# Optimization experiments

Hardware: AMD Instinct MI355X
Metric: run time of the kernel (lower is better)

## Reference

```python
import jax, jax.numpy as jnp
import numpy as np
from jax import lax

T, B = 32, 32
GRID = (16, 16)
N_ACT = 5
CNN_DIM = 512
MAP_DIM = CNN_DIM + N_ACT  # 517
FLAT = MAP_DIM * GRID[0] * GRID[1]  # 132352


def _conv(x, w, b, stride):
    y = lax.conv_general_dilated(x, w, (stride, stride), 'VALID',
                                 dimension_numbers=('NCHW', 'OIHW', 'NCHW'))
    return jax.nn.relu(y + b[None, :, None, None])


def setup_inputs() -> dict:
    key = jax.random.key(0)
    ks = jax.random.split(key, 16)
    inp = {
        'image': jax.random.uniform(ks[0], (T * B, 3, 64, 64), jnp.float32),
        'last_action': jax.random.randint(ks[1], (T * B,), 0, N_ACT),
        'position': jax.random.randint(ks[2], (T * B, 2), 0, GRID[0]),
        'done': jnp.zeros((T, B), jnp.float32),
        'state0': jnp.zeros((B, MAP_DIM, GRID[0], GRID[1]), jnp.float32),
        'c1_w': jax.random.normal(ks[3], (32, 3, 8, 8), jnp.float32) * 0.05,
        'c1_b': jnp.zeros((32,), jnp.float32),
        'c2_w': jax.random.normal(ks[4], (64, 32, 4, 4), jnp.float32) * 0.05,
        'c2_b': jnp.zeros((64,), jnp.float32),
        'c3_w': jax.random.normal(ks[5], (64, 64, 3, 3), jnp.float32) * 0.05,
        'c3_b': jnp.zeros((64,), jnp.float32),
        'fc_w': jax.random.normal(ks[6], (CNN_DIM, 1024), jnp.float32) * 0.03,
        'fc_b': jnp.zeros((CNN_DIM,), jnp.float32),
        'pol_w1': jax.random.normal(ks[7], (64, FLAT), jnp.float32) * 0.005,
        'pol_b1': jnp.zeros((64,), jnp.float32),
        'pol_w2': jax.random.normal(ks[8], (N_ACT, 64), jnp.float32) * 0.01,
        'pol_b2': jnp.zeros((N_ACT,), jnp.float32),
        'val_w1': jax.random.normal(ks[9], (64, FLAT), jnp.float32) * 0.005,
        'val_b1': jnp.zeros((64,), jnp.float32),
        'val_w2': jax.random.normal(ks[10], (1, 64), jnp.float32) * 0.01,
        'val_b2': jnp.zeros((1,), jnp.float32),
    }
    return inp


def reference(image, last_action, position, done, state0,
              c1_w, c1_b, c2_w, c2_b, c3_w, c3_b, fc_w, fc_b,
              pol_w1, pol_b1, pol_w2, pol_b2, val_w1, val_b1, val_w2, val_b2):
    # NatureCNN feature extractor (image already normalized to [0,1])
    x = _conv(image, c1_w, c1_b, 4)   # (TB,32,15,15)
    x = _conv(x, c2_w, c2_b, 2)       # (TB,64,6,6)
    x = _conv(x, c3_w, c3_b, 1)       # (TB,64,4,4)
    feat = jax.nn.relu(x.reshape(x.shape[0], -1) @ fc_w.T + fc_b)  # (TB,512)
    onehot = jax.nn.one_hot(last_action, N_ACT, dtype=feat.dtype)
    h = jnp.concatenate([feat, onehot], axis=1)       # (TB,517)

    h_seq = h.reshape(T, B, MAP_DIM)
    idx_seq = position.reshape(T, B, 2)
    benv = jnp.arange(B)

    def step(state, inp):
        ht, dt, it = inp
        masked = (1.0 - dt)[:, None, None, None] * state      # reset done envs
        new_state = masked.at[benv, :, it[:, 0], it[:, 1]].set(ht)  # scatter write
        return new_state, new_state.reshape(B, -1)

    final_state, outs = lax.scan(step, state0, (h_seq, done, idx_seq))
    hidden = outs.reshape(T * B, FLAT)

    logits = jnp.tanh(hidden @ pol_w1.T + pol_b1) @ pol_w2.T + pol_b2  # (TB,5)
    v = jnp.tanh(hidden @ val_w1.T + val_b1) @ val_w2.T + val_b2       # (TB,1)
    return logits, v, final_state
```

## Files before the change

kernel.cpp:

```cpp
#include <hip/hip_runtime.h>

#define T_ 32
#define B_ 32
#define MAPD 517
#define P_ 256
#define FLATD (MAPD*P_)
#define TBN (T_*B_)

typedef unsigned short u16;
typedef unsigned int u32;
typedef __attribute__((ext_vector_type(4))) short short4v;
typedef __attribute__((ext_vector_type(8))) short short8v;
typedef __attribute__((ext_vector_type(4))) float f32x4;
typedef __attribute__((ext_vector_type(2))) float f32x2;
typedef __attribute__((ext_vector_type(4))) u32 u32x4;

__device__ __forceinline__ float bfv(u16 u){ u32 x = ((u32)u)<<16; return __uint_as_float(x); }
__device__ __forceinline__ u16 fbf(float f){
  u32 x = __float_as_uint(f);
  return (u16)((x + 0x7fffu + ((x>>16)&1u))>>16);
}
template<bool F32> __device__ __forceinline__ float ld(const void* p, size_t i){
  if constexpr (F32) return ((const float*)p)[i];
  else               return bfv(((const u16*)p)[i]);
}
__device__ __forceinline__ float ldf(bool f32, const void* p, size_t i){
  return f32 ? ((const float*)p)[i] : bfv(((const u16*)p)[i]);
}

__device__ __forceinline__ bool probe_f32(const void* img){
  int lane = threadIdx.x & 63;
  ushort4 v = ((const ushort4*)img)[lane];
  int c = (v.x <= 0x4380u) + (v.y <= 0x4380u) + (v.z <= 0x4380u) + (v.w <= 0x4380u);
  #pragma unroll
  for (int off = 32; off > 0; off >>= 1) c += __shfl_xor(c, off, 64);
  return c < 240;
}

template<bool F32> __device__ void wt_body(int lbid, const void* pw1, const void* vw1,
                                           u16* wt, u32* tile){
  int c  = lbid >> 1;
  int ph = lbid & 1;
  for (int half = 0; half < 2; ++half){
    for (int it = 0; it < 2; ++it){
      int idx = it*256 + threadIdx.x;
      int jp = idx >> 3, pgl = idx & 7;
      int j0 = jp*2;
      const void* w = (j0 < 64) ? pw1 : vw1;
      int jj0 = (j0 < 64) ? j0 : j0-64;
      size_t base0 = (size_t)jj0*FLATD + c*P_ + ph*128 + half*64 + pgl*8;
      size_t base1 = base0 + FLATD;
      u16 a[8], b[8];
      if constexpr (F32){
        const float* f = (const float*)w;
        float4 a0 = *(const float4*)(f + base0), a1 = *(const float4*)(f + base0 + 4);
        float4 b0 = *(const float4*)(f + base1), b1 = *(const float4*)(f + base1 + 4);
        a[0]=fbf(a0.x); a[1]=fbf(a0.y); a[2]=fbf(a0.z); a[3]=fbf(a0.w);
        a[4]=fbf(a1.x); a[5]=fbf(a1.y); a[6]=fbf(a1.z); a[7]=fbf(a1.w);
        b[0]=fbf(b0.x); b[1]=fbf(b0.y); b[2]=fbf(b0.z); b[3]=fbf(b0.w);
        b[4]=fbf(b1.x); b[5]=fbf(b1.y); b[6]=fbf(b1.z); b[7]=fbf(b1.w);
      } else {
        short8v va = *(const short8v*)((const u16*)w + base0);
        short8v vb = *(const short8v*)((const u16*)w + base1);
        #pragma unroll
        for (int k = 0; k < 8; ++k){ a[k] = (u16)va[k]; b[k] = (u16)vb[k]; }
      }
      int slot = (jp >> 2) ^ (half*8 + pgl);
      int sub  = jp & 3;
      #pragma unroll
      for (int k = 0; k < 8; ++k){
        int ppl = pgl*8 + k;
        tile[ppl*64 + slot*4 + sub] = (u32)a[k] | ((u32)b[k] << 16);
      }
    }
    __syncthreads();
    for (int it = 0; it < 4; ++it){
      int idx = it*256 + threadIdx.x;
      int ppl = idx >> 4, jb = idx & 15;
      int slot = jb ^ (half*8 + (ppl >> 3));
      u32x4 v = *(const u32x4*)(tile + ppl*64 + slot*4);
      int p = ph*128 + half*64 + ppl;
      *(u32x4*)(wt + ((size_t)p*MAPD + c)*128 + jb*8) = v;
    }
    __syncthreads();
  }
}

__device__ void prep_body(bool f32, int bid, const void* c1w, const void* c2w, const void* c3w,
                          const void* fcw, const void* st0,
                          u16* W1F, u16* W2F, u16* W3F, u16* FWF, u16* ST0T, char* smem_){
  int tid = threadIdx.x;
  if (bid < 24){
    int idx = bid*256 + tid;
    int j = idx & 7, l = (idx>>3) & 63, t = idx>>9;
    int nt = t/6, s = t - nt*6;
    int oc = nt*16 + (l&15);
    int kk = 8*(4*s + (l>>4)) + j;
    float v = ldf(f32, c1w, oc*192+kk);
    W1F[idx] = fbf(v);
  } else if (bid < 152){
    int idx = (bid-24)*256 + tid;
    int j = idx & 7, l = (idx>>3) & 63, s = (idx>>9) & 15, nt = idx>>13;
    int oc = nt*16 + (l&15);
    int cin = (l>>4)*8 + j;
    int src = oc*512 + cin*16 + (s>>2)*4 + (s&3);
    W2F[idx] = fbf(ldf(f32, c2w, src));
  } else if (bid < 296){
    int idx = (bid-152)*256 + tid;
    int j = idx & 7, l = (idx>>3) & 63, t = idx>>9;
    int nt = t/18, s = t - nt*18;
    int oc = nt*16 + (l&15);
    int c = (s&1)*32 + (l>>4)*8 + j;
    int src = oc*576 + c*9 + (s>>1);
    W3F[idx] = fbf(ldf(f32, c3w, src));
  } else if (bid < 328){
    u16* tile = (u16*)smem_;
    int nt = bid - 296;
    int ol = tid >> 4;
    int o  = nt*16 + ol;
    for (int par = 0; par < 2; ++par){
      for (int it = 0; it < 2; ++it){
        int m = par*32 + it*16 + (tid & 15);
        int col = (((m>>3)&3)*16 + ol)*8 + (m&7);
        u16 v[16];
        if (f32){
          const float* f = (const float*)fcw + (size_t)o*1024 + 16*m;
          #pragma unroll
          for (int q = 0; q < 4; ++q){
            float4 x = *(const float4*)(f + q*4);
            v[q*4+0]=fbf(x.x); v[q*4+1]=fbf(x.y); v[q*4+2]=fbf(x.z); v[q*4+3]=fbf(x.w);
          }
        } else {
          const u16* f = (const u16*)fcw + (size_t)o*1024 + 16*m;
          short8v x0 = *(const short8v*)f;
          short8v x1 = *(const short8v*)(f + 8);
          #pragma unroll
          for (int q = 0; q < 8; ++q){ v[q] = (u16)x0[q]; v[8+q] = (u16)x1[q]; }
        }
        #pragma unroll
        for (int r = 0; r < 16; ++r)
          tile[r*512 + col] = v[r];
      }
      __syncthreads();
      for (int it = 0; it < 4; ++it){
        int idx = it*256 + tid;
        int row = idx >> 6, colv = idx & 63;
        u32x4 w = *(const u32x4*)((const u32*)tile + row*256 + colv*4);
        int frag = nt*32 + row*2 + par;
        *(u32x4*)(FWF + (size_t)frag*512 + colv*8) = w;
      }
      __syncthreads();
    }
  } else {
    u16* tile = (u16*)smem_;
    int b0 = bid - 328;
    int c0 = (b0 >> 2)*8, p0 = (b0 & 3)*64;
    for (int half = 0; half < 2; ++half){
      int ch = c0 + half*4;
      for (int it = 0; it < 4; ++it){
        int idx = it*256 + tid;
        int pg = idx & 7, b = (idx>>3) & 31, ci = idx >> 8;
        int c = ch + ci;
        u16 v[8];
        if (c < MAPD){
          size_t src = ((size_t)b*MAPD + c)*256 + p0 + pg*8;
          if (f32){
            const float* f = (const float*)st0;
            float4 x0 = *(const float4*)(f + src), x1 = *(const float4*)(f + src + 4);
            v[0]=fbf(x0.x); v[1]=fbf(x0.y); v[2]=fbf(x0.z); v[3]=fbf(x0.w);
            v[4]=fbf(x1.x); v[5]=fbf(x1.y); v[6]=fbf(x1.z); v[7]=fbf(x1.w);
          } else {
            short8v x = *(const short8v*)((const u16*)st0 + src);
            #pragma unroll
            for (int k = 0; k < 8; ++k) v[k] = (u16)x[k];
          }
        } else {
          #pragma unroll
          for (int k = 0; k < 8; ++k) v[k] = 0;
        }
        #pragma unroll
        for (int kk = 0; kk < 8; ++kk){
          int k2 = (kk + pg) & 7;
          tile[ci*2304 + (pg*8 + k2)*36 + b] = v[k2];
        }
      }
      __syncthreads();
      for (int it = 0; it < 8; ++it){
        int idx = it*256 + tid;
        int bq = idx & 7, pl = (idx>>3) & 63, ci = idx >> 9;
        int c = ch + ci;
        if (c < MAPD){
          ushort4 v = *(const ushort4*)(tile + ci*2304 + pl*36 + bq*4);
          *(ushort4*)(ST0T + ((size_t)(p0+pl)*MAPD + c)*32 + bq*4) = v;
        }
      }
      __syncthreads();
    }
  }
}

__device__ void meta_body(bool f32, int bid, const int* pos, const void* done, const int* lact,
                          int* prev, float* coef, float* H, int* lastw, float* lastc){
  if (bid < 4){
    int i = bid*256 + threadIdx.x;
    int t = i >> 5, b = i & 31;
    int p = pos[i*2]*16 + pos[i*2+1];
    int pv = -1;
    for (int s = t-1; s >= 0; --s){
      int n = s*32 + b;
      if (pos[n*2]*16 + pos[n*2+1] == p){ pv = s; break; }
    }
    float cf = 1.f;
    for (int s = (pv<0?0:pv+1); s <= t-1; ++s)
      cf *= (1.f - ldf(f32, done, s*32+b));
    prev[i] = pv; coef[i] = cf;
    int la = lact[i];
    #pragma unroll
    for (int a = 0; a < 5; ++a) H[(size_t)i*MAPD + 512 + a] = (la == a) ? 1.f : 0.f;
  } else {
    int i = (bid-4)*256 + threadIdx.x;
    int b = i >> 8, p = i & 255;
    int lw = -1;
    for (int s = T_-1; s >= 0; --s){
      int n = s*32 + b;
      if (pos[n*2]*16 + pos[n*2+1] == p){ lw = s; break; }
    }
    float cf = 1.f;
    for (int s = (lw<0?0:lw+1); s < T_; ++s)
      cf *= (1.f - ldf(f32, done, s*32+b));
    lastw[i] = lw; lastc[i] = cf;
  }
}

__global__ __launch_bounds__(256) void k_A(const void* image,
                                           const void* pw1, const void* vw1, u16* wt,
                                           const void* c1w, const void* c2w, const void* c3w,
                                           const void* fcw, const void* st0,
                                           u16* W1F, u16* W2F, u16* W3F, u16* FWF, u16* ST0T,
                                           const int* pos, const void* done, const int* lact,
                                           int* prev, float* coef, float* H, int* lastw, float* lastc){
  __shared__ __align__(16) char smem_[18464];
  bool f32 = probe_f32(image);
  int bid = blockIdx.x;
  if (bid < 1034){
    if (f32) wt_body<true>(bid, pw1, vw1, wt, (u32*)smem_);
    else     wt_body<false>(bid, pw1, vw1, wt, (u32*)smem_);
  } else if (bid < 1622){
    prep_body(f32, bid-1034, c1w, c2w, c3w, fcw, st0, W1F, W2F, W3F, FWF, ST0T, smem_);
  } else {
    meta_body(f32, bid-1622, pos, done, lact, prev, coef, H, lastw, lastc);
  }
}

__global__ __launch_bounds__(256) void k_conv123(const void* img,
                                                 const u16* __restrict__ W1F, const void* b1,
                                                 const u16* __restrict__ W2F, const void* b2,
                                                 const u16* __restrict__ W3F, const void* b3,
                                                 u16* __restrict__ out){
  __shared__ __align__(16) u16 smem[19488];
  u16* sImg = smem;
  u16* sA   = smem + 12288;
  u16* sBv  = smem;
  bool f32 = probe_f32(img);
  int n = blockIdx.x, tid = threadIdx.x;
  if (f32){
    const float4* ip = (const float4*)((const float*)img + (size_t)n*12288);
    for (int i = tid; i < 3072; i += 256){
      float4 v = ip[i];
      ushort4 u; u.x = fbf(v.x); u.y = fbf(v.y); u.z = fbf(v.z); u.w = fbf(v.w);
      int L = i*4;
      int addr = (L & ~63) | (((L & 63) + (((L >> 6) & 3) << 4)) & 63);
      *(ushort4*)(sImg + addr) = u;
    }
  } else {
    const ushort4* ip = (const ushort4*)((const u16*)img + (size_t)n*12288);
    for (int i = tid; i < 3072; i += 256){
      ushort4 u = ip[i];
      int L = i*4;
      int addr = (L & ~63) | (((L & 63) + (((L >> 6) & 3) << 4)) & 63);
      *(ushort4*)(sImg + addr) = u;
    }
  }
  int wv = tid >> 6, lane = tid & 63;
  int mi = lane & 15, q = lane >> 4;

  short8v bfr1[2][6];
  #pragma unroll
  for (int nt = 0; nt < 2; ++nt)
    #pragma unroll
    for (int s = 0; s < 6; ++s)
      bfr1[nt][s] = ((const short8v*)W1F)[(nt*6+s)*64 + lane];
  float b1v[2];
  #pragma unroll
  for (int nt = 0; nt < 2; ++nt)
    b1v[nt] = ldf(f32, b1, nt*16+mi);
  __syncthreads();

  {
    f32x4 acc[4][2];
    #pragma unroll
    for (int mt = 0; mt < 4; ++mt)
      #pragma unroll
      for (int nt = 0; nt < 2; ++nt)
        acc[mt][nt] = (f32x4){0.f,0.f,0.f,0.f};
    int base[4];
    #pragma unroll
    for (int mt = 0; mt < 4; ++mt){
      int m = (wv*4+mt)*16 + mi;
      int mc = m < 225 ? m : 224;
      int oy = mc/15, ox = mc - oy*15;
      base[mt] = oy*256 + ox*4;
    }
    for (int s = 0; s < 6; ++s){
      int cky = 4*s + q;
      int off = (cky >> 3)*4096 + (cky & 7)*64;
      #pragma unroll
      for (int mt = 0; mt < 4; ++mt){
        int Lb = base[mt] + off;
        const u16* rp = sImg + (Lb & ~63);
        int x0 = Lb & 63;
        int rot = ((Lb >> 6) & 3) << 4;
        short4v lo = *(const short4v*)(rp + ((x0 + rot) & 63));
        short4v hi = *(const short4v*)(rp + ((x0 + 4 + rot) & 63));
        short8v a = __builtin_shufflevector(lo, hi, 0,1,2,3,4,5,6,7);
        acc[mt][0] = __builtin_amdgcn_mfma_f32_16x16x32_bf16(a, bfr1[0][s], acc[mt][0], 0,0,0);
        acc[mt][1] = __builtin_amdgcn_mfma_f32_16x16x32_bf16(a, bfr1[1][s], acc[mt][1], 0,0,0);
      }
    }
    __syncthreads();
    #pragma unroll
    for (int mt = 0; mt < 4; ++mt){
      int mrow0 = (wv*4+mt)*16 + q*4;
      #pragma unroll
      for (int nt = 0; nt < 2; ++nt){
        int oc = nt*16 + mi;
        #pragma unroll
        for (int r = 0; r < 4; ++r){
          int m = mrow0 + r;
          if (m < 225){
            int g = ((oc >> 3) ^ ((m >> 1) & 3)) << 3;
            sA[m*32 + g + (oc & 7)] = fbf(fmaxf(acc[mt][nt][r] + b1v[nt], 0.f));
          }
        }
      }
    }
  }
  __syncthreads();

  {
    short8v bfr2[16];
    #pragma unroll
    for (int s = 0; s < 16; ++s)
      bfr2[s] = ((const short8v*)W2F)[(wv*16+s)*64 + lane];
    int oc = wv*16 + mi;
    float bv = ldf(f32, b2, oc);
    f32x4 acc[3];
    #pragma unroll
    for (int mt = 0; mt < 3; ++mt) acc[mt] = (f32x4){0.f,0.f,0.f,0.f};
    int pixb[3];
    #pragma unroll
    for (int mt = 0; mt < 3; ++mt){
      int m = mt*16 + mi; if (m > 35) m = 35;
      int oy = m/6, ox = m - oy*6;
      pixb[mt] = oy*30 + ox*2;
    }
    #pragma unroll
    for (int s = 0; s < 16; ++s){
      int dp = (s>>2)*15 + (s&3);
      #pragma unroll
      for (int mt = 0; mt < 3; ++mt){
        int pix = pixb[mt] + dp;
        int g = (q ^ ((pix >> 1) & 3)) << 3;
        short8v a = *(const short8v*)(sA + pix*32 + g);
        acc[mt] = __builtin_amdgcn_mfma_f32_16x16x32_bf16(a, bfr2[s], acc[mt], 0,0,0);
      }
    }
    __syncthreads();
    #pragma unroll
    for (int mt = 0; mt < 3; ++mt)
      #pragma unroll
      for (int r = 0; r < 4; ++r){
        int m = mt*16 + q*4 + r;
        if (m < 36){
          int g = ((oc >> 3) ^ (m & 7)) << 3;
          sBv[m*64 + g + (oc & 7)] = fbf(fmaxf(acc[mt][r] + bv, 0.f));
        }
      }
  }
  __syncthreads();

  {
    int oy = mi >> 2, ox = mi & 3;
    int oc = wv*16 + mi;
    float bv = ldf(f32, b3, oc);
    short8v bfr3[18];
    #pragma unroll
    for (int s = 0; s < 18; ++s)
      bfr3[s] = ((const short8v*)W3F)[(wv*18+s)*64 + lane];
    f32x4 acc = (f32x4){0.f,0.f,0.f,0.f};
    #pragma unroll
    for (int s = 0; s < 18; ++s){
      int pair = s >> 1, ky = pair/3, kx = pair - ky*3;
      int pix = (oy+ky)*6 + ox+kx;
      int g = ((((s & 1) << 2) | q) ^ (pix & 7)) << 3;
      short8v a = *(const short8v*)(sBv + pix*64 + g);
      acc = __builtin_amdgcn_mfma_f32_16x16x32_bf16(a, bfr3[s], acc, 0,0,0);
    }
    u16* ob = out + (size_t)n*1024;
    #pragma unroll
    for (int r = 0; r < 4; ++r)
      ob[(q*4+r)*64 + oc] = fbf(fmaxf(acc[r] + bv, 0.f));
  }
}

template<int CLEN>
__device__ __forceinline__ void yloop(const u16* __restrict__ wp, const float* __restrict__ sSb,
                                      float (&acc)[8][2]){
  #pragma unroll 10
  for (int c = 0; c < CLEN; ++c){
    u32 w = *(const u32*)(wp + (size_t)c*128);
    float w0 = bfv((u16)(w & 0xffffu)), w1 = bfv((u16)(w >> 16));
    const float4* s4 = (const float4*)(sSb + c*32);
    float4 sa = s4[0], sb = s4[1];
    float sv[8] = {sa.x,sa.y,sa.z,sa.w,sb.x,sb.y,sb.z,sb.w};
    #pragma unroll
    for (int bb = 0; bb < 8; ++bb){
      acc[bb][0] += sv[bb]*w0;
      acc[bb][1] += sv[bb]*w1;
    }
  }
}
__device__ void yinit_body(int lbid, const u16* __restrict__ ST0T, const u16* __restrict__ wt,
                           u16* __restrict__ PARTB, float* sS){
  int p = lbid >> 2, cq = lbid & 3;
  int c0 = cq*130;
  int clen = (cq == 3) ? 127 : 130;
  const ushort4* ssrc = (const ushort4*)(ST0T + ((size_t)p*MAPD + c0)*32);
  int n4 = clen*8;
  for (int i = threadIdx.x; i < n4; i += 256){
    ushort4 u = ssrc[i];
    float4 f; f.x = bfv(u.x); f.y = bfv(u.y); f.z = bfv(u.z); f.w = bfv(u.w);
    *(float4*)(sS + i*4) = f;
  }
  __syncthreads();
  int jg = threadIdx.x & 63, bg = threadIdx.x >> 6;
  int j0 = jg*2, b0 = bg*8;
  const u16* wp = wt + ((size_t)p*MAPD + c0)*128 + j0;
  float acc[8][2] = {};
  if (cq < 3) yloop<130>(wp, sS + b0, acc);
  else        yloop<127>(wp, sS + b0, acc);
  u32* op = (u32*)(PARTB + (size_t)lbid*4096);
  #pragma unroll
  for (int bb = 0; bb < 8; ++bb){
    u32 pk = (u32)fbf(acc[bb][0]) | ((u32)fbf(acc[bb][1]) << 16);
    op[((b0+bb)*128 + j0) >> 1] = pk;
  }
}
__device__ void fc_body(int lbid, bool f32, const u16* __restrict__ C, const u16* __restrict__ FWF,
                        const void* fb, float* __restrict__ H){
  int wv = threadIdx.x >> 6, lane = threadIdx.x & 63;
  int mi = lane & 15, q = lane >> 4;
  int mt = lbid >> 3;
  int nt = (lbid & 7)*4 + wv;
  const u16* ap = C + (size_t)(mt*16 + mi)*1024 + q*8;
  const short8v* bp = (const short8v*)FWF + (size_t)nt*32*64 + lane;
  f32x4 acc0 = (f32x4){0.f,0.f,0.f,0.f};
  f32x4 acc1 = (f32x4){0.f,0.f,0.f,0.f};
  #pragma unroll
  for (int kt = 0; kt < 32; kt += 2){
    short8v a0 = *(const short8v*)(ap + kt*32);
    short8v b0 = bp[kt*64];
    short8v a1 = *(const short8v*)(ap + (kt+1)*32);
    short8v b1 = bp[(kt+1)*64];
    acc0 = __builtin_amdgcn_mfma_f32_16x16x32_bf16(a0, b0, acc0, 0,0,0);
    acc1 = __builtin_amdgcn_mfma_f32_16x16x32_bf16(a1, b1, acc1, 0,0,0);
  }
  int o = nt*16 + mi;
  float bv = ldf(f32, fb, o);
  #pragma unroll
  for (int r = 0; r < 4; ++r){
    int m = mt*16 + q*4 + r;
    H[(size_t)m*MAPD + o] = fmaxf(acc0[r] + acc1[r] + bv, 0.f);
  }
}
__global__ __launch_bounds__(256) void k_C(const void* image,
                                           const u16* __restrict__ ST0T, const u16* __restrict__ wt,
                                           u16* __restrict__ PARTB,
                                           const u16* __restrict__ C, const u16* __restrict__ FWF,
                                           const void* fb, float* __restrict__ H){
  __shared__ float sS[130*32];
  if (blockIdx.x < 1024){
    yinit_body(blockIdx.x, ST0T, wt, PARTB, sS);
  } else {
    bool f32 = probe_f32(image);
    fc_body(blockIdx.x - 1024, f32, C, FWF, fb, H);
  }
}

__device__ void delta_body(int obid, int ltid, float* diff, bool f32,
                           const float* __restrict__ H, const u16* __restrict__ wt,
                           const u16* __restrict__ st0t,
                           const int* __restrict__ pos, const void* done,
                           const int* __restrict__ prev, const float* __restrict__ coef,
                           float* __restrict__ dlt8){
  int n = obid >> 2, cq = obid & 3;
  int c0 = cq*130, clen = (cq == 3) ? 127 : 130;
  int b = n & 31;
  int p = pos[n*2]*16 + pos[n*2+1];
  float dn = ldf(f32, done, n);
  float m = 1.f - dn;
  int pv = prev[n];
  float cf = coef[n]*m;
  const float* hc = H + (size_t)n*MAPD + c0;
  for (int c = ltid; c < clen; c += 128){
    float old;
    if (pv >= 0) old = H[(size_t)(pv*32 + b)*MAPD + c0 + c];
    else         old = bfv(st0t[((size_t)p*MAPD + c0 + c)*32 + b]);
    diff[c] = hc[c] - cf*old;
  }
  __syncthreads();
  int half = ltid >> 6, jp = ltid & 63, j0 = jp*2;
  int hbase, hlen;
  if (cq == 3){ hbase = half*64; hlen = half ? 63 : 64; }
  else        { hbase = half*65; hlen = 65; }
  const u16* wp = wt + ((size_t)p*MAPD + c0 + hbase)*128 + j0;
  const float* dptr = diff + hbase;
  float a0 = 0.f, a1 = 0.f;
  int c = 0;
  for (; c + 4 <= hlen; c += 4){
    u32 w0 = *(const u32*)(wp + (size_t)(c+0)*128);
    u32 w1 = *(const u32*)(wp + (size_t)(c+1)*128);
    u32 w2 = *(const u32*)(wp + (size_t)(c+2)*128);
    u32 w3 = *(const u32*)(wp + (size_t)(c+3)*128);
    float d0 = dptr[c], d1 = dptr[c+1], d2 = dptr[c+2], d3 = dptr[c+3];
    a0 += d0*bfv((u16)(w0 & 0xffffu)) + d1*bfv((u16)(w1 & 0xffffu))
        + d2*bfv((u16)(w2 & 0xffffu)) + d3*bfv((u16)(w3 & 0xffffu));
    a1 += d0*bfv((u16)(w0 >> 16)) + d1*bfv((u16)(w1 >> 16))
        + d2*bfv((u16)(w2 >> 16)) + d3*bfv((u16)(w3 >> 16));
  }
  for (; c < hlen; ++c){
    u32 w = *(const u32*)(wp + (size_t)c*128);
    a0 += dptr[c]*bfv((u16)(w & 0xffffu));
    a1 += dptr[c]*bfv((u16)(w >> 16));
  }
  f32x2 st; st[0] = a0; st[1] = a1;
  *(f32x2*)(dlt8 + ((size_t)obid*2 + half)*128 + j0) = st;
}
__global__ __launch_bounds__(256) void k_D(const void* image,
                                           const float* __restrict__ H, const u16* __restrict__ wt,
                                           const u16* __restrict__ st0t,
                                           const int* __restrict__ pos, const void* done,
                                           const int* __restrict__ prev, const float* __restrict__ coef,
                                           float* __restrict__ dlt8,
                                           const u16* __restrict__ PARTB, float* __restrict__ YI){
  __shared__ float diff2[2][132];
  __shared__ float red[256];
  if (blockIdx.x < 2048){
    bool f32 = probe_f32(image);
    int sub = threadIdx.x >> 7;
    int obid = blockIdx.x*2 + sub;
    delta_body(obid, threadIdx.x & 127, diff2[sub], f32, H, wt, st0t, pos, done, prev, coef, dlt8);
  } else {
    int lbid = blockIdx.x - 2048;
    int o = lbid*64 + (threadIdx.x & 63);
    int kq = threadIdx.x >> 6;
    float s = 0.f;
    const u16* pp = PARTB + (size_t)kq*256*4096 + o;
    #pragma unroll 8
    for (int k = 0; k < 256; ++k) s += bfv(pp[(size_t)k*4096]);
    red[threadIdx.x] = s;
    __syncthreads();
    if (threadIdx.x < 64)
      YI[o] = red[threadIdx.x] + red[threadIdx.x+64] + red[threadIdx.x+128] + red[threadIdx.x+192];
  }
}

__device__ void scan_heads_body(bool f32, const float* __restrict__ yi,
                                const float* __restrict__ dlt8, const void* done,
                                const void* pb1, const void* vb1,
                                const void* pw2, const void* pb2,
                                const void* vw2, const void* vb2, void* out,
                                float* sd, float* sm){
  int b = blockIdx.x;
  for (int it = 0; it < 16; ++it){
    int idx = it*256 + threadIdx.x;
    int t = idx >> 7, j = idx & 127;
    const float* dp = dlt8 + (size_t)(t*32 + b)*1024 + j;
    sd[idx] = dp[0] + dp[128] + dp[256] + dp[384]
            + dp[512] + dp[640] + dp[768] + dp[896];
  }
  if (threadIdx.x < 32) sm[threadIdx.x] = 1.f - ldf(f32, done, threadIdx.x*32 + b);
  __syncthreads();
  if (threadIdx.x >= 128) return;
  int j = threadIdx.x;
  int lane = j & 63;
  bool pol = j < 64;
  float y = yi[b*128 + j];
  float bias = pol ? ldf(f32, pb1, j) : ldf(f32, vb1, j-64);
  float w2[5];
  if (pol){
    #pragma unroll
    for (int jj = 0; jj < 5; ++jj) w2[jj] = ldf(f32, pw2, jj*64 + lane);
  } else {
    w2[0] = ldf(f32, vw2, lane);
  }
  for (int t = 0; t < T_; ++t){
    int n = t*32 + b;
    y = sm[t]*y + sd[t*128 + j];
    float th = tanhf(y + bias);
    if (pol){
      float s0 = th*w2[0], s1 = th*w2[1], s2 = th*w2[2], s3 = th*w2[3], s4 = th*w2[4];
      #pragma unroll
      for (int off = 32; off > 0; off >>= 1){
        s0 += __shfl_xor(s0, off, 64);
        s1 += __shfl_xor(s1, off, 64);
        s2 += __shfl_xor(s2, off, 64);
        s3 += __shfl_xor(s3, off, 64);
        s4 += __shfl_xor(s4, off, 64);
      }
      if (lane == 0){
        float sv[5] = {s0,s1,s2,s3,s4};
        #pragma unroll
        for (int jj = 0; jj < 5; ++jj){
          float s = sv[jj] + ldf(f32, pb2, jj);
          if (f32) ((float*)out)[n*5 + jj] = s; else ((u16*)out)[n*5 + jj] = fbf(s);
        }
      }
    } else {
      float s = th*w2[0];
      #pragma unroll
      for (int off = 32; off > 0; off >>= 1) s += __shfl_xor(s, off, 64);
      if (lane == 0){
        s += ldf(f32, vb2, 0);
        if (f32) ((float*)out)[5120 + n] = s; else ((u16*)out)[5120 + n] = fbf(s);
      }
    }
  }
}
__global__ __launch_bounds__(256) void k_E(const void* image,
                                           const float* __restrict__ yi, const float* __restrict__ dlt8,
                                           const void* done, const void* pb1, const void* vb1,
                                           const void* pw2, const void* pb2,
                                           const void* vw2, const void* vb2,
                                           const float* __restrict__ H, const void* st0,
                                           const int* __restrict__ lastw, const float* __restrict__ lastc,
                                           void* out){
  __shared__ float sd[32*128];
  __shared__ float sm[32];
  bool f32 = probe_f32(image);
  if (blockIdx.x < 32){
    scan_heads_body(f32, yi, dlt8, done, pb1, vb1, pw2, pb2, vw2, vb2, out, sd, sm);
  } else {
    size_t i0 = (size_t)(blockIdx.x - 32)*2048 + (size_t)threadIdx.x*8;
    int b = (int)(i0 / FLATD);
    int r = (int)(i0 - (size_t)b*FLATD);
    int c = r >> 8, p0 = r & 255;
    int4 lwa = *(const int4*)(lastw + b*256 + p0);
    int4 lwb = *(const int4*)(lastw + b*256 + p0 + 4);
    float4 lca = *(const float4*)(lastc + b*256 + p0);
    float4 lcb = *(const float4*)(lastc + b*256 + p0 + 4);
    int   lw[8] = {lwa.x,lwa.y,lwa.z,lwa.w,lwb.x,lwb.y,lwb.z,lwb.w};
    float lc[8] = {lca.x,lca.y,lca.z,lca.w,lcb.x,lcb.y,lcb.z,lcb.w};
    float v[8];
    if (f32){
      float4 s0 = *(const float4*)((const float*)st0 + i0);
      float4 s1 = *(const float4*)((const float*)st0 + i0 + 4);
      v[0]=s0.x; v[1]=s0.y; v[2]=s0.z; v[3]=s0.w;
      v[4]=s1.x; v[5]=s1.y; v[6]=s1.z; v[7]=s1.w;
    } else {
      short8v s = *(const short8v*)((const u16*)st0 + i0);
      #pragma unroll
      for (int k = 0; k < 8; ++k) v[k] = bfv((u16)s[k]);
    }
    #pragma unroll
    for (int k = 0; k < 8; ++k){
      if (lw[k] >= 0) v[k] = H[(size_t)(lw[k]*32 + b)*MAPD + c];
      v[k] *= lc[k];
    }
    if (f32){
      float4 o0 = {v[0],v[1],v[2],v[3]}, o1 = {v[4],v[5],v[6],v[7]};
      float* op = (float*)out + 6144 + i0;
      *(float4*)op = o0; *(float4*)(op+4) = o1;
    } else {
      ushort4 o0, o1;
      o0.x=fbf(v[0]); o0.y=fbf(v[1]); o0.z=fbf(v[2]); o0.w=fbf(v[3]);
      o1.x=fbf(v[4]); o1.y=fbf(v[5]); o1.z=fbf(v[6]); o1.w=fbf(v[7]);
      u16* op = (u16*)out + 6144 + i0;
      *(ushort4*)op = o0; *(ushort4*)(op+4) = o1;
    }
  }
}

extern "C" void kernel_launch(void* const* d_in, const int* in_sizes, int n_in,
                              void* d_out, int out_size, void* d_ws, size_t ws_size,
                              hipStream_t stream) {
  (void)in_sizes; (void)n_in; (void)out_size; (void)ws_size;
  const void* image = d_in[0];
  const int*  lact  = (const int*)d_in[1];
  const int*  pos   = (const int*)d_in[2];
  const void* done  = d_in[3];
  const void* st0   = d_in[4];
  const void* c1w = d_in[5];  const void* c1b = d_in[6];
  const void* c2w = d_in[7];  const void* c2b = d_in[8];
  const void* c3w = d_in[9];  const void* c3b = d_in[10];
  const void* fcw = d_in[11]; const void* fcb = d_in[12];
  const void* pw1 = d_in[13]; const void* pb1 = d_in[14];
  const void* pw2 = d_in[15]; const void* pb2 = d_in[16];
  const void* vw1 = d_in[17]; const void* vb1 = d_in[18];
  const void* vw2 = d_in[19]; const void* vb2 = d_in[20];
  char* ws = (char*)d_ws;

  u16*   WT    = (u16*)  (ws + 0);
  float* H     = (float*)(ws + 33882368);
  float* YI    = (float*)(ws + 36000256);
  u16*   PARTB = (u16*)  (ws + 36016640);
  int*   PREV  = (int*)  (ws + 44405248);
  float* COEF  = (float*)(ws + 44409344);
  int*   LASTW = (int*)  (ws + 44413440);
  float* LASTC = (float*)(ws + 44446208);
  u16*   W1F   = (u16*)  (ws + 44479232);
  u16*   W2F   = (u16*)  (ws + 44491520);
  u16*   W3F   = (u16*)  (ws + 44557056);
  u16*   FWF   = (u16*)  (ws + 44630784);
  u16*   ST0T  = (u16*)  (ws + 45679360);
  u16*   C     = (u16*)  (ws + 54149888);
  float* DLT8  = (float*)(ws + 56247040);

  k_A      <<<1658, 256, 0, stream>>>(image, pw1, vw1, WT, c1w, c2w, c3w, fcw, st0,
                                      W1F, W2F, W3F, FWF, ST0T,
                                      pos, done, lact, PREV, COEF, H, LASTW, LASTC);
  k_conv123<<<1024, 256, 0, stream>>>(image, W1F, c1b, W2F, c2b, W3F, c3b, C);
  k_C      <<<1536, 256, 0, stream>>>(image, ST0T, WT, PARTB, C, FWF, fcb, H);
  k_D      <<<2112, 256, 0, stream>>>(image, H, WT, ST0T, pos, done, PREV, COEF, DLT8, PARTB, YI);
  k_E      <<<2100, 256, 0, stream>>>(image, YI, DLT8, done, pb1, vb1, pw2, pb2, vw2, vb2,
                                      H, st0, LASTW, LASTC, d_out);
}
```

Before: 317.2 us.

## Compute initial-state head projection with MFMA split-K GEMM in first kernel

```diff
diff --git a/kernel.cpp b/kernel.cpp
--- a/kernel.cpp
+++ b/kernel.cpp
@@ -26,6 +26,17 @@
 }
 __device__ __forceinline__ float ldf(bool f32, const void* p, size_t i){
   return f32 ? ((const float*)p)[i] : bfv(((const u16*)p)[i]);
+}
+__device__ __forceinline__ short8v ldfrag(bool f32, const void* p, size_t off){
+  if (f32){
+    const float* f = (const float*)p + off;
+    float4 x0 = *(const float4*)f, x1 = *(const float4*)(f + 4);
+    short8v r;
+    r[0]=(short)fbf(x0.x); r[1]=(short)fbf(x0.y); r[2]=(short)fbf(x0.z); r[3]=(short)fbf(x0.w);
+    r[4]=(short)fbf(x1.x); r[5]=(short)fbf(x1.y); r[6]=(short)fbf(x1.z); r[7]=(short)fbf(x1.w);
+    return r;
+  }
+  return *(const short8v*)((const u16*)p + off);
 }
 
 __device__ __forceinline__ bool probe_f32(const void* img){
@@ -232,13 +243,54 @@
   }
 }
 
+__device__ void yinit_gemm(int bk, bool f32, const void* pw1, const void* vw1,
+                           const void* st0, float* __restrict__ YIP){
+  int wv = threadIdx.x >> 6, lane = threadIdx.x & 63;
+  int mi = lane & 15, q = lane >> 4;
+  int k0 = bk*1056;
+  int nsteps = (bk < 125) ? 33 : 11;
+  int j0 = wv*32;
+  const void* wA; int jA = j0 + mi;
+  const void* wB; int jB = j0 + 16 + mi;
+  if (jA < 64){ wA = pw1; } else { wA = vw1; jA -= 64; }
+  if (jB < 64){ wB = pw1; } else { wB = vw1; jB -= 64; }
+  f32x4 acc[2][2];
+  #pragma unroll
+  for (int mt = 0; mt < 2; ++mt)
+    #pragma unroll
+    for (int jt = 0; jt < 2; ++jt) acc[mt][jt] = (f32x4){0.f,0.f,0.f,0.f};
+  for (int s = 0; s < nsteps; ++s){
+    size_t kk = (size_t)k0 + s*32 + q*8;
+    short8v a0 = ldfrag(f32, st0, (size_t)(0*16 + mi)*FLATD + kk);
+    short8v a1 = ldfrag(f32, st0, (size_t)(1*16 + mi)*FLATD + kk);
+    short8v b0 = ldfrag(f32, wA, (size_t)jA*FLATD + kk);
+    short8v b1 = ldfrag(f32, wB, (size_t)jB*FLATD + kk);
+    acc[0][0] = __builtin_amdgcn_mfma_f32_16x16x32_bf16(a0, b0, acc[0][0], 0,0,0);
+    acc[0][1] = __builtin_amdgcn_mfma_f32_16x16x32_bf16(a0, b1, acc[0][1], 0,0,0);
+    acc[1][0] = __builtin_amdgcn_mfma_f32_16x16x32_bf16(a1, b0, acc[1][0], 0,0,0);
+    acc[1][1] = __builtin_amdgcn_mfma_f32_16x16x32_bf16(a1, b1, acc[1][1], 0,0,0);
+  }
+  float* op = YIP + (size_t)bk*4096;
+  #pragma unroll
+  for (int mt = 0; mt < 2; ++mt)
+    #pragma unroll
+    for (int jt = 0; jt < 2; ++jt)
+      #pragma unroll
+      for (int r = 0; r < 4; ++r){
+        int b = mt*16 + q*4 + r;
+        int j = j0 + jt*16 + mi;
+        op[b*128 + j] = acc[mt][jt][r];
+      }
+}
+
 __global__ __launch_bounds__(256) void k_A(const void* image,
                                            const void* pw1, const void* vw1, u16* wt,
                                            const void* c1w, const void* c2w, const void* c3w,
                                            const void* fcw, const void* st0,
                                            u16* W1F, u16* W2F, u16* W3F, u16* FWF, u16* ST0T,
                                            const int* pos, const void* done, const int* lact,
-                                           int* prev, float* coef, float* H, int* lastw, float* lastc){
+                                           int* prev, float* coef, float* H, int* lastw, float* lastc,
+                                           float* YIP){
   __shared__ __align__(16) char smem_[18464];
   bool f32 = probe_f32(image);
   int bid = blockIdx.x;
@@ -247,8 +299,10 @@
     else     wt_body<false>(bid, pw1, vw1, wt, (u32*)smem_);
   } else if (bid < 1622){
     prep_body(f32, bid-1034, c1w, c2w, c3w, fcw, st0, W1F, W2F, W3F, FWF, ST0T, smem_);
+  } else if (bid < 1658){
+    meta_body(f32, bid-1622, pos, done, lact, prev, coef, H, lastw, lastc);
   } else {
-    meta_body(f32, bid-1622, pos, done, lact, prev, coef, H, lastw, lastc);
+    yinit_gemm(bid-1658, f32, pw1, vw1, st0, YIP);
   }
 }
 
@@ -256,8 +310,23 @@
                                                  const u16* __restrict__ W1F, const void* b1,
                                                  const u16* __restrict__ W2F, const void* b2,
                                                  const u16* __restrict__ W3F, const void* b3,
-                                                 u16* __restrict__ out){
+                                                 u16* __restrict__ out,
+                                                 const float* __restrict__ YIP, float* __restrict__ YI){
   __shared__ __align__(16) u16 smem[19488];
+  if (blockIdx.x >= 1024){
+    float* red = (float*)smem;
+    int lbid = blockIdx.x - 1024;
+    int o = lbid*64 + (threadIdx.x & 63);
+    int kq = threadIdx.x >> 6;
+    int kbeg = kq*32, kend = (kq == 3) ? 126 : (kbeg + 32);
+    float s = 0.f;
+    for (int k = kbeg; k < kend; ++k) s += YIP[(size_t)k*4096 + o];
+    red[threadIdx.x] = s;
+    __syncthreads();
+    if (threadIdx.x < 64)
+      YI[o] = red[threadIdx.x] + red[threadIdx.x+64] + red[threadIdx.x+128] + red[threadIdx.x+192];
+    return;
+  }
   u16* sImg = smem;
   u16* sA   = smem + 12288;
   u16* sBv  = smem;
@@ -413,55 +482,14 @@
   }
 }
 
-template<int CLEN>
-__device__ __forceinline__ void yloop(const u16* __restrict__ wp, const float* __restrict__ sSb,
-                                      float (&acc)[8][2]){
-  #pragma unroll 10
-  for (int c = 0; c < CLEN; ++c){
-    u32 w = *(const u32*)(wp + (size_t)c*128);
-    float w0 = bfv((u16)(w & 0xffffu)), w1 = bfv((u16)(w >> 16));
-    const float4* s4 = (const float4*)(sSb + c*32);
-    float4 sa = s4[0], sb = s4[1];
-    float sv[8] = {sa.x,sa.y,sa.z,sa.w,sb.x,sb.y,sb.z,sb.w};
-    #pragma unroll
-    for (int bb = 0; bb < 8; ++bb){
-      acc[bb][0] += sv[bb]*w0;
-      acc[bb][1] += sv[bb]*w1;
-    }
-  }
-}
-__device__ void yinit_body(int lbid, const u16* __restrict__ ST0T, const u16* __restrict__ wt,
-                           u16* __restrict__ PARTB, float* sS){
-  int p = lbid >> 2, cq = lbid & 3;
-  int c0 = cq*130;
-  int clen = (cq == 3) ? 127 : 130;
-  const ushort4* ssrc = (const ushort4*)(ST0T + ((size_t)p*MAPD + c0)*32);
-  int n4 = clen*8;
-  for (int i = threadIdx.x; i < n4; i += 256){
-    ushort4 u = ssrc[i];
-    float4 f; f.x = bfv(u.x); f.y = bfv(u.y); f.z = bfv(u.z); f.w = bfv(u.w);
-    *(float4*)(sS + i*4) = f;
-  }
-  __syncthreads();
-  int jg = threadIdx.x & 63, bg = threadIdx.x >> 6;
-  int j0 = jg*2, b0 = bg*8;
-  const u16* wp = wt + ((size_t)p*MAPD + c0)*128 + j0;
-  float acc[8][2] = {};
-  if (cq < 3) yloop<130>(wp, sS + b0, acc);
-  else        yloop<127>(wp, sS + b0, acc);
-  u32* op = (u32*)(PARTB + (size_t)lbid*4096);
-  #pragma unroll
-  for (int bb = 0; bb < 8; ++bb){
-    u32 pk = (u32)fbf(acc[bb][0]) | ((u32)fbf(acc[bb][1]) << 16);
-    op[((b0+bb)*128 + j0) >> 1] = pk;
-  }
-}
-__device__ void fc_body(int lbid, bool f32, const u16* __restrict__ C, const u16* __restrict__ FWF,
-                        const void* fb, float* __restrict__ H){
+__global__ __launch_bounds__(256) void k_C(const void* image,
+                                           const u16* __restrict__ C, const u16* __restrict__ FWF,
+                                           const void* fb, float* __restrict__ H){
+  bool f32 = probe_f32(image);
   int wv = threadIdx.x >> 6, lane = threadIdx.x & 63;
   int mi = lane & 15, q = lane >> 4;
-  int mt = lbid >> 3;
-  int nt = (lbid & 7)*4 + wv;
+  int mt = blockIdx.x >> 3;
+  int nt = (blockIdx.x & 7)*4 + wv;
   const u16* ap = C + (size_t)(mt*16 + mi)*1024 + q*8;
   const short8v* bp = (const short8v*)FWF + (size_t)nt*32*64 + lane;
   f32x4 acc0 = (f32x4){0.f,0.f,0.f,0.f};
@@ -481,19 +509,6 @@
   for (int r = 0; r < 4; ++r){
     int m = mt*16 + q*4 + r;
     H[(size_t)m*MAPD + o] = fmaxf(acc0[r] + acc1[r] + bv, 0.f);
-  }
-}
-__global__ __launch_bounds__(256) void k_C(const void* image,
-                                           const u16* __restrict__ ST0T, const u16* __restrict__ wt,
-                                           u16* __restrict__ PARTB,
-                                           const u16* __restrict__ C, const u16* __restrict__ FWF,
-                                           const void* fb, float* __restrict__ H){
-  __shared__ float sS[130*32];
-  if (blockIdx.x < 1024){
-    yinit_body(blockIdx.x, ST0T, wt, PARTB, sS);
-  } else {
-    bool f32 = probe_f32(image);
-    fc_body(blockIdx.x - 1024, f32, C, FWF, fb, H);
   }
 }
 
@@ -551,28 +566,12 @@
                                            const u16* __restrict__ st0t,
                                            const int* __restrict__ pos, const void* done,
                                            const int* __restrict__ prev, const float* __restrict__ coef,
-                                           float* __restrict__ dlt8,
-                                           const u16* __restrict__ PARTB, float* __restrict__ YI){
+                                           float* __restrict__ dlt8){
   __shared__ float diff2[2][132];
-  __shared__ float red[256];
-  if (blockIdx.x < 2048){
-    bool f32 = probe_f32(image);
-    int sub = threadIdx.x >> 7;
-    int obid = blockIdx.x*2 + sub;
-    delta_body(obid, threadIdx.x & 127, diff2[sub], f32, H, wt, st0t, pos, done, prev, coef, dlt8);
-  } else {
-    int lbid = blockIdx.x - 2048;
-    int o = lbid*64 + (threadIdx.x & 63);
-    int kq = threadIdx.x >> 6;
-    float s = 0.f;
-    const u16* pp = PARTB + (size_t)kq*256*4096 + o;
-    #pragma unroll 8
-    for (int k = 0; k < 256; ++k) s += bfv(pp[(size_t)k*4096]);
-    red[threadIdx.x] = s;
-    __syncthreads();
-    if (threadIdx.x < 64)
-      YI[o] = red[threadIdx.x] + red[threadIdx.x+64] + red[threadIdx.x+128] + red[threadIdx.x+192];
-  }
+  bool f32 = probe_f32(image);
+  int sub = threadIdx.x >> 7;
+  int obid = blockIdx.x*2 + sub;
+  delta_body(obid, threadIdx.x & 127, diff2[sub], f32, H, wt, st0t, pos, done, prev, coef, dlt8);
 }
 
 __device__ void scan_heads_body(bool f32, const float* __restrict__ yi,
@@ -713,7 +712,7 @@
   u16*   WT    = (u16*)  (ws + 0);
   float* H     = (float*)(ws + 33882368);
   float* YI    = (float*)(ws + 36000256);
-  u16*   PARTB = (u16*)  (ws + 36016640);
+  float* YIP   = (float*)(ws + 36016640);
   int*   PREV  = (int*)  (ws + 44405248);
   float* COEF  = (float*)(ws + 44409344);
   int*   LASTW = (int*)  (ws + 44413440);
@@ -726,12 +725,12 @@
   u16*   C     = (u16*)  (ws + 54149888);
   float* DLT8  = (float*)(ws + 56247040);
 
-  k_A      <<<1658, 256, 0, stream>>>(image, pw1, vw1, WT, c1w, c2w, c3w, fcw, st0,
+  k_A      <<<1784, 256, 0, stream>>>(image, pw1, vw1, WT, c1w, c2w, c3w, fcw, st0,
                                       W1F, W2F, W3F, FWF, ST0T,
-                                      pos, done, lact, PREV, COEF, H, LASTW, LASTC);
-  k_conv123<<<1024, 256, 0, stream>>>(image, W1F, c1b, W2F, c2b, W3F, c3b, C);
-  k_C      <<<1536, 256, 0, stream>>>(image, ST0T, WT, PARTB, C, FWF, fcb, H);
-  k_D      <<<2112, 256, 0, stream>>>(image, H, WT, ST0T, pos, done, PREV, COEF, DLT8, PARTB, YI);
+                                      pos, done, lact, PREV, COEF, H, LASTW, LASTC, YIP);
+  k_conv123<<<1088, 256, 0, stream>>>(image, W1F, c1b, W2F, c2b, W3F, c3b, C, YIP, YI);
+  k_C      <<<512, 256, 0, stream>>>(image, C, FWF, fcb, H);
+  k_D      <<<2048, 256, 0, stream>>>(image, H, WT, ST0T, pos, done, PREV, COEF, DLT8);
   k_E      <<<2100, 256, 0, stream>>>(image, YI, DLT8, done, pb1, vb1, pw2, pb2, vw2, vb2,
                                       H, st0, LASTW, LASTC, d_out);
 }
```

New measurement: 342.8 us. 8.1% more time.
